# Kernel tuning notes

Measured on AMD Instinct MI355X. Metric: run time of the kernel, lower is better.

Reference implementation:

```python
import jax, jax.numpy as jnp
import numpy as np

ATT_WIDTH = 512  # attention_width from init

def _band_mask(T, width, dtype):
    # tf.matrix_band_part(ones, width//2, (width-1)//2): keep i-j<=lower and j-i<=upper
    lower = width // 2
    upper = (width - 1) // 2
    i = jnp.arange(T)[:, None]
    j = jnp.arange(T)[None, :]
    keep = (i - j <= lower) & (j - i <= upper)
    return keep.astype(dtype)

def setup_inputs() -> dict:
    key = jax.random.key(0)
    k1, k2, k3, k4 = jax.random.split(key, 4)
    B, T, H, D = 8, 2048, 1024, 1024
    scale = 1.0 / np.sqrt(H)  # keep activations sane
    return {
        "inputs": jax.random.normal(k1, (B, T, H), dtype=jnp.float32),
        "WQ": jax.random.normal(k2, (H, D), dtype=jnp.float32) * scale,
        "WK": jax.random.normal(k3, (H, D), dtype=jnp.float32) * scale,
        "WV": jax.random.normal(k4, (H, D), dtype=jnp.float32) * scale,
    }

def reference(inputs, WQ, WK, WV) -> jnp.ndarray:
    B, T, H = inputs.shape
    D = WQ.shape[1]
    scale = jnp.asarray(D, inputs.dtype) ** 0.5
    q = jnp.einsum('bth,hd->btd', inputs, WQ)
    k = jnp.einsum('bth,hd->btd', inputs, WK)
    v = jnp.einsum('bth,hd->btd', inputs, WV)
    score = jnp.einsum('bqd,bkd->bqk', q, k) / scale  # [B,T,T]
    # NOTE: original multiplies score by the 0/1 band mask BEFORE softmax
    # (masked entries become 0, not -inf). Faithful reproduction.
    local = _band_mask(T, ATT_WIDTH, score.dtype)
    score = score * local[None, :, :]
    attn = jax.nn.softmax(score, axis=-1)
    return jnp.einsum('bqk,bkd->bqd', attn, v)
```

## Files before the change

kernel.cpp:

```cpp
#include <hip/hip_runtime.h>
#include <hip/hip_bf16.h>
#include <stdint.h>

typedef __attribute__((ext_vector_type(8))) short bf16x8;
typedef __attribute__((ext_vector_type(4))) short short4v;
typedef __attribute__((ext_vector_type(4))) float f32x4;

#define DEV static __device__ __forceinline__

DEV float bf2f(short u) {
    union { float f; uint32_t i; } c; c.i = ((uint32_t)(uint16_t)u) << 16; return c.f;
}
DEV short f2bf(float f) {
    union { float f; uint32_t i; } c; c.f = f;
    uint32_t i = c.i;
    uint32_t r = i + 0x7FFFu + ((i >> 16) & 1u);
    return (short)(r >> 16);
}

DEV void gload_lds16(const short* g, short* l) {
    __builtin_amdgcn_global_load_lds(
        (const __attribute__((address_space(1))) void*)g,
        (__attribute__((address_space(3))) void*)l,
        16, 0, 0);
}

__global__ __launch_bounds__(256)
void cvt_f32_bf16(const float* __restrict__ in, short* __restrict__ out) {
    long i = ((long)blockIdx.x * 256 + threadIdx.x) * 8;
    float4 a = *(const float4*)&in[i];
    float4 b = *(const float4*)&in[i + 4];
    bf16x8 o;
    o[0] = f2bf(a.x); o[1] = f2bf(a.y); o[2] = f2bf(a.z); o[3] = f2bf(a.w);
    o[4] = f2bf(b.x); o[5] = f2bf(b.y); o[6] = f2bf(b.z); o[7] = f2bf(b.w);
    *(bf16x8*)&out[i] = o;
}

__global__ __launch_bounds__(256)
void transpose_w(const float* __restrict__ W, short* __restrict__ Wt) {
    const int HD = 1024;
    __shared__ float tile[32][33];
    int bx = blockIdx.x, by = blockIdx.y;
    int tx = threadIdx.x & 31, ty = threadIdx.x >> 5;
    #pragma unroll
    for (int r = ty; r < 32; r += 8)
        tile[r][tx] = W[(long)(by * 32 + r) * HD + bx * 32 + tx];
    __syncthreads();
    #pragma unroll
    for (int r = ty; r < 32; r += 8)
        Wt[(long)(bx * 32 + r) * HD + by * 32 + tx] = f2bf(tile[tx][r]);
}


DEV void stage_half(const short* __restrict__ src, int ld, short* dst, int tid) {
    int rr = tid >> 3;
    int cs = ((tid & 7) ^ (rr & 7)) << 3;
    short* d = dst + ((tid >> 6) << 9);
    gload_lds16(src + (long)rr * ld + cs, d);
    gload_lds16(src + (long)(rr + 64) * ld + cs, d + 4096);
}

DEV bf16x8 ld_frag(const short* half, int rowbase, int ks, int lane) {
    int row = rowbase + (lane & 15);
    int idx = (row << 6) + ks * 32 + ((lane >> 4) << 3);
    idx ^= (lane & 7) << 3;
    return *(const bf16x8*)&half[idx];
}

#define SB   __builtin_amdgcn_s_barrier()
#define SCHED0 __builtin_amdgcn_sched_barrier(0)
#define LGK0 do { asm volatile("s_waitcnt lgkmcnt(0)" ::: "memory"); SCHED0; } while (0)
#define VM(n) asm volatile("s_waitcnt vmcnt(" #n ")" ::: "memory")
#define PRIO1 __builtin_amdgcn_s_setprio(1)
#define PRIO0 __builtin_amdgcn_s_setprio(0)

#define READ_A(HP, QM)                                                          \
    do { _Pragma("unroll") for (int iq = 0; iq < 4; ++iq)                       \
         _Pragma("unroll") for (int ks = 0; ks < 2; ++ks)                       \
             ra[iq][ks] = ld_frag(HP, (QM)*64 + iq*16, ks, lane); } while (0)

#define READ_B(HP, QN)                                                          \
    do { _Pragma("unroll") for (int jn = 0; jn < 2; ++jn)                       \
         _Pragma("unroll") for (int ks = 0; ks < 2; ++ks)                       \
             rb[QN][jn][ks] = ld_frag(HP, wn1*64 + (QN)*32 + jn*16, ks, lane); } while (0)

#define MFMA_Q(QM, QN)                                                          \
    do { _Pragma("unroll") for (int iq = 0; iq < 4; ++iq)                       \
         _Pragma("unroll") for (int jn = 0; jn < 2; ++jn)                       \
         _Pragma("unroll") for (int ks = 0; ks < 2; ++ks)                       \
             acc[(QM)*4+iq][(QN)*2+jn] = __builtin_amdgcn_mfma_f32_16x16x32_bf16( \
                 ra[iq][ks], rb[QN][jn][ks], acc[(QM)*4+iq][(QN)*2+jn], 0,0,0); } while (0)

template<int EPI>
__global__ __launch_bounds__(512, 2)
void gemm256(const short* __restrict__ Abase, const short* __restrict__ Bbase,
             void* __restrict__ o0, void* __restrict__ o1, void* __restrict__ o2,
             const float* __restrict__ Crow, const float* __restrict__ Vsum)
{
    const int T = 2048, HD = 1024;
    __shared__ __align__(16) short lds[2][2][2][8192];

    const int tid  = threadIdx.x;
    const int lane = tid & 63;
    const int w    = tid >> 6;
    const int wm   = w >> 2;
    const int wn   = w & 3;
    const int wn1  = wn & 1;
    const int bz   = blockIdx.z;

    int m0, n0, klo, khi, ldA, ldB;
    const short *A, *B;
    if (EPI == 0) {
        m0 = blockIdx.y * 256; n0 = blockIdx.x * 256;
        klo = 0; khi = 1024; ldA = HD; ldB = HD;
        A = Abase; B = Bbase;
    } else if (EPI == 1) {
        int mb = blockIdx.y, kb = mb + (int)blockIdx.x - 1;
        if (kb < 0 || kb > 7) return;
        m0 = mb * 256; n0 = kb * 256;
        klo = 0; khi = 1024; ldA = HD; ldB = HD;
        A = Abase + (long)bz * T * HD; B = Bbase + (long)bz * T * HD;
    } else {
        int mb = blockIdx.y;
        m0 = mb * 256; n0 = blockIdx.x * 256;
        klo = max(m0 - 256, 0); khi = min(m0 + 512, T);
        ldA = T; ldB = T;
        A = Abase + (long)bz * T * T; B = Bbase + (long)bz * HD * T;
    }

    const short* Asrc = A + (long)m0 * ldA + klo;
    const short* Bsrc = B + (long)n0 * ldB + klo;
    const short* hA0 = &lds[0][0][wm][0];
    const short* hA1 = &lds[1][0][wm][0];
    const short* hB0 = &lds[0][1][wn >> 1][0];
    const short* hB1 = &lds[1][1][wn >> 1][0];

    auto stA = [&](int bf, int hf, int t) {
        stage_half(Asrc + (long)hf * 128 * ldA + t * 64, ldA, (short*)&lds[bf][0][hf][0], tid); };
    auto stB = [&](int bf, int hf, int t) {
        stage_half(Bsrc + (long)hf * 128 * ldB + t * 64, ldB, (short*)&lds[bf][1][hf][0], tid); };

    f32x4 acc[8][4];
    #pragma unroll
    for (int i = 0; i < 8; ++i)
        #pragma unroll
        for (int j = 0; j < 4; ++j) { acc[i][j][0]=0.f; acc[i][j][1]=0.f; acc[i][j][2]=0.f; acc[i][j][3]=0.f; }
    bf16x8 ra[4][2];
    bf16x8 rb[2][2][2];

    const int NT = (khi - klo) >> 6;

    stB(0,0,0); stB(0,1,0); stA(0,0,0); stA(0,1,0); stB(1,0,1); stB(1,1,1);
    SCHED0; VM(4); SB;

    for (int i = 0; i < NT/2 - 1; ++i) {
        int t1 = 2*i+1, t2 = 2*i+2, t3 = 2*i+3;
        READ_A(hA0,0); READ_B(hB0,0); stA(1,0,t1); SCHED0; SB; LGK0; PRIO1; MFMA_Q(0,0); PRIO0; SB; SCHED0;
        READ_B(hB0,1); stA(1,1,t1); SCHED0; SB; LGK0; PRIO1; MFMA_Q(0,1); PRIO0; SB; SCHED0;
        READ_A(hA0,1); stB(0,0,t2); SCHED0; SB; LGK0; PRIO1; MFMA_Q(1,1); PRIO0; SB; SCHED0;
        stB(0,1,t2); SCHED0; SB; LGK0; PRIO1; MFMA_Q(1,0); PRIO0; VM(4); SB; SCHED0;
        READ_A(hA1,0); READ_B(hB1,0); stA(0,0,t2); SCHED0; SB; LGK0; PRIO1; MFMA_Q(0,0); PRIO0; SB; SCHED0;
        READ_B(hB1,1); stA(0,1,t2); SCHED0; SB; LGK0; PRIO1; MFMA_Q(0,1); PRIO0; SB; SCHED0;
        READ_A(hA1,1); stB(1,0,t3); SCHED0; SB; LGK0; PRIO1; MFMA_Q(1,1); PRIO0; SB; SCHED0;
        stB(1,1,t3); SCHED0; SB; LGK0; PRIO1; MFMA_Q(1,0); PRIO0; VM(4); SB; SCHED0;
    }
    {
        int t1 = NT - 1;
        READ_A(hA0,0); READ_B(hB0,0); stA(1,0,t1); SCHED0; SB; LGK0; PRIO1; MFMA_Q(0,0); PRIO0; SB; SCHED0;
        READ_B(hB0,1); stA(1,1,t1); SCHED0; SB; LGK0; PRIO1; MFMA_Q(0,1); PRIO0; SB; SCHED0;
        READ_A(hA0,1); SCHED0; SB; LGK0; PRIO1; MFMA_Q(1,1); PRIO0; SB; SCHED0;
        SB; LGK0; PRIO1; MFMA_Q(1,0); PRIO0; VM(0); SB; SCHED0;
        READ_A(hA1,0); READ_B(hB1,0); SCHED0; SB; LGK0; PRIO1; MFMA_Q(0,0); PRIO0; SB; SCHED0;
        READ_B(hB1,1); SCHED0; SB; LGK0; PRIO1; MFMA_Q(0,1); PRIO0; SB; SCHED0;
        READ_A(hA1,1); SCHED0; SB; LGK0; PRIO1; MFMA_Q(1,1); PRIO0; SB; SCHED0;
        SB; LGK0; PRIO1; MFMA_Q(1,0); PRIO0;
    }

    const int fr = lane & 15, fq = lane >> 4;
    const int rbase = m0 + wm * 128, cbase = n0 + wn * 64;

    if (EPI == 0) {
        const int wsel = n0 >> 10;
        if (wsel < 2) {
            short* dst = (short*)(wsel ? o1 : o0);
            #pragma unroll
            for (int mi = 0; mi < 8; ++mi)
                #pragma unroll
                for (int ni = 0; ni < 4; ++ni)
                    #pragma unroll
                    for (int r = 0; r < 4; ++r) {
                        int row = rbase + mi * 16 + fq * 4 + r;
                        int col = (cbase + ni * 16 + fr) & 1023;
                        dst[(long)row * HD + col] = f2bf(acc[mi][ni][r]);
                    }
        } else {
            short* Vt = (short*)o2;
            #pragma unroll
            for (int mi = 0; mi < 8; ++mi)
                #pragma unroll
                for (int ni = 0; ni < 4; ++ni) {
                    int col  = (cbase + ni * 16 + fr) & 1023;
                    int row0 = rbase + mi * 16 + fq * 4;
                    int b = row0 >> 11, t = row0 & 2047;
                    short4v v;
                    #pragma unroll
                    for (int r = 0; r < 4; ++r) v[r] = f2bf(acc[mi][ni][r]);
                    *(short4v*)&Vt[((long)b * HD + col) * T + t] = v;
                }
        }
    } else if (EPI == 1) {
        short* S = (short*)o0 + (long)bz * T * T;
        #pragma unroll
        for (int mi = 0; mi < 8; ++mi)
            #pragma unroll
            for (int ni = 0; ni < 4; ++ni)
                #pragma unroll
                for (int r = 0; r < 4; ++r) {
                    int i = rbase + mi * 16 + fq * 4 + r;
                    int j = cbase + ni * 16 + fr;
                    bool keep = (i - j <= 256) && (j - i <= 255);
                    S[(long)i * T + j] = f2bf(keep ? acc[mi][ni][r] * (1.f/32.f) : 0.f);
                }
    } else {
        float* out = (float*)o0;
        #pragma unroll
        for (int mi = 0; mi < 8; ++mi)
            #pragma unroll
            for (int r = 0; r < 4; ++r) {
                int i = rbase + mi * 16 + fq * 4 + r;
                float ci = Crow[bz * T + i];
                #pragma unroll
                for (int ni = 0; ni < 4; ++ni) {
                    int col = cbase + ni * 16 + fr;
                    out[((long)bz * T + i) * HD + col] = acc[mi][ni][r] + ci * Vsum[bz * HD + col];
                }
            }
    }
}

__global__ __launch_bounds__(256)
void softmax_band(short* __restrict__ S, float* __restrict__ Crow) {
    const int T = 2048;
    int wid = (int)blockIdx.x * 4 + (threadIdx.x >> 6);
    int lane = threadIdx.x & 63;
    int b = wid >> 11, t = wid & 2047;
    int mb = t >> 7;
    int tlo = max(mb - 2, 0) * 128;
    int thi = min(mb + 2, 15) * 128 + 128;
    int nvec = (thi - tlo) >> 3;
    short* row = S + ((long)b * T + t) * T + tlo;

    bool h0 = lane < nvec;
    bool h1 = lane + 64 < nvec;
    bf16x8 v0, v1;
    float f0[8], f1[8];
    float m = 0.f;
    if (h0) {
        v0 = *(const bf16x8*)&row[lane * 8];
        #pragma unroll
        for (int j = 0; j < 8; ++j) { f0[j] = bf2f(v0[j]); m = fmaxf(m, f0[j]); }
    }
    if (h1) {
        v1 = *(const bf16x8*)&row[(lane + 64) * 8];
        #pragma unroll
        for (int j = 0; j < 8; ++j) { f1[j] = bf2f(v1[j]); m = fmaxf(m, f1[j]); }
    }
    #pragma unroll
    for (int o = 32; o; o >>= 1) m = fmaxf(m, __shfl_xor(m, o));

    float e0[8], e1[8];
    float sum = 0.f;
    if (h0) {
        #pragma unroll
        for (int j = 0; j < 8; ++j) { e0[j] = __expf(f0[j] - m); sum += e0[j]; }
    }
    if (h1) {
        #pragma unroll
        for (int j = 0; j < 8; ++j) { e1[j] = __expf(f1[j] - m); sum += e1[j]; }
    }
    #pragma unroll
    for (int o = 32; o; o >>= 1) sum += __shfl_xor(sum, o);
    float em = __expf(-m);
    sum += (float)(2048 - nvec * 8) * em;
    float inv = 1.f / sum;
    float c = em * inv;

    if (h0) {
        #pragma unroll
        for (int j = 0; j < 8; ++j) v0[j] = f2bf(e0[j] * inv - c);
        *(bf16x8*)&row[lane * 8] = v0;
    }
    if (h1) {
        #pragma unroll
        for (int j = 0; j < 8; ++j) v1[j] = f2bf(e1[j] * inv - c);
        *(bf16x8*)&row[(lane + 64) * 8] = v1;
    }
    if (lane == 0) Crow[wid] = c;
}

__global__ __launch_bounds__(256)
void vsum_rows(const short* __restrict__ Vt, float* __restrict__ Vsum) {
    int rowid = (int)blockIdx.x * 4 + (threadIdx.x >> 6);
    int lane = threadIdx.x & 63;
    const short* r = Vt + (long)rowid * 2048;
    float s = 0.f;
    #pragma unroll
    for (int v = 0; v < 4; ++v) {
        bf16x8 x = *(const bf16x8*)&r[(lane + v * 64) * 8];
        #pragma unroll
        for (int j = 0; j < 8; ++j) s += bf2f(x[j]);
    }
    #pragma unroll
    for (int o = 32; o; o >>= 1) s += __shfl_xor(s, o);
    if (lane == 0) Vsum[rowid] = s;
}

extern "C" void kernel_launch(void* const* d_in, const int* in_sizes, int n_in,
                              void* d_out, int out_size, void* d_ws, size_t ws_size,
                              hipStream_t stream) {
    const int B = 8, T = 2048, H = 1024, D = 1024;
    const long MT = (long)B * T;

    const float* X  = (const float*)d_in[0];
    const float* WQ = (const float*)d_in[1];
    const float* WK = (const float*)d_in[2];
    const float* WV = (const float*)d_in[3];
    float* out = (float*)d_out;

    char* ws = (char*)d_ws;
    size_t off = 0;
    auto alloc = [&](size_t bytes) {
        char* p = ws + off;
        off += (bytes + 255) & ~(size_t)255;
        return p;
    };
    short* Xb   = (short*)alloc(MT * H * 2);
    short* Wt   = (short*)alloc(3L * D * H * 2);
    short* Qb   = (short*)alloc(MT * D * 2);
    short* Kb   = (short*)alloc(MT * D * 2);
    short* Vt   = (short*)alloc((long)B * D * T * 2);
    short* S    = (short*)alloc((long)B * T * T * 2);
    float* Crow = (float*)alloc(MT * 4);
    float* Vsum = (float*)alloc((long)B * D * 4);
    if (off > ws_size) return;

    cvt_f32_bf16<<<(int)(MT * H / 2048), 256, 0, stream>>>(X, Xb);
    transpose_w<<<dim3(32, 32), 256, 0, stream>>>(WQ, Wt);
    transpose_w<<<dim3(32, 32), 256, 0, stream>>>(WK, Wt + (long)D * H);
    transpose_w<<<dim3(32, 32), 256, 0, stream>>>(WV, Wt + 2L * D * H);

    gemm256<0><<<dim3(12, 64, 1), 512, 0, stream>>>(Xb, Wt, Qb, Kb, Vt, nullptr, nullptr);

    vsum_rows<<<(int)(B * D / 4), 256, 0, stream>>>(Vt, Vsum);

    gemm256<1><<<dim3(3, 8, B), 512, 0, stream>>>(Qb, Kb, S, nullptr, nullptr, nullptr, nullptr);

    softmax_band<<<(int)(MT / 4), 256, 0, stream>>>(S, Crow);

    gemm256<2><<<dim3(4, 8, B), 512, 0, stream>>>(S, Vt, out, nullptr, nullptr, Crow, Vsum);
}
```

Baseline: 254.3 us.

## Halve barriers in GEMM pipeline and remap blocks for XCD-aware scheduling

Rewrites the main loop schedule so each quarter-step uses one barrier instead of two. B fragments for the next quadrant are prefetched before the barrier, and partial lgkmcnt/vmcnt waits let LDS reads overlap MFMAs. It also remaps linear block IDs so blocks sharing a batch or tile land on the same XCD (p&7), aiming for better L2 reuse. The finer waits and swapped MFMA quadrant order add risk of LDS races if the counts are wrong.

```diff
diff --git a/kernel.cpp b/kernel.cpp
--- a/kernel.cpp
+++ b/kernel.cpp
@@ -67,10 +67,10 @@
     return *(const bf16x8*)&half[idx];
 }
 
-#define SB   __builtin_amdgcn_s_barrier()
 #define SCHED0 __builtin_amdgcn_sched_barrier(0)
-#define LGK0 do { asm volatile("s_waitcnt lgkmcnt(0)" ::: "memory"); SCHED0; } while (0)
-#define VM(n) asm volatile("s_waitcnt vmcnt(" #n ")" ::: "memory")
+#define SBAR do { SCHED0; __builtin_amdgcn_s_barrier(); SCHED0; } while (0)
+#define LGK(n) do { asm volatile("s_waitcnt lgkmcnt(" #n ")" ::: "memory"); SCHED0; } while (0)
+#define VM(n)  do { asm volatile("s_waitcnt vmcnt(" #n ")" ::: "memory"); SCHED0; } while (0)
 #define PRIO1 __builtin_amdgcn_s_setprio(1)
 #define PRIO0 __builtin_amdgcn_s_setprio(0)
 
@@ -106,23 +106,28 @@
     const int wm   = w >> 2;
     const int wn   = w & 3;
     const int wn1  = wn & 1;
-    const int bz   = blockIdx.z;
-
-    int m0, n0, klo, khi, ldA, ldB;
+
+    int m0, n0, klo, khi, ldA, ldB, bz;
     const short *A, *B;
     if (EPI == 0) {
-        m0 = blockIdx.y * 256; n0 = blockIdx.x * 256;
-        klo = 0; khi = 1024; ldA = HD; ldB = HD;
+        int p = (int)blockIdx.x + 12 * (int)blockIdx.y;
+        int lid = (p & 7) * 96 + (p >> 3);
+        m0 = (lid / 12) * 256; n0 = (lid % 12) * 256;
+        klo = 0; khi = 1024; ldA = HD; ldB = HD; bz = 0;
         A = Abase; B = Bbase;
     } else if (EPI == 1) {
-        int mb = blockIdx.y, kb = mb + (int)blockIdx.x - 1;
+        int p = (int)blockIdx.x + 3 * ((int)blockIdx.y + 8 * (int)blockIdx.z);
+        bz = p & 7; int rem = p >> 3;
+        int mb = rem / 3, kb = mb + rem % 3 - 1;
         if (kb < 0 || kb > 7) return;
         m0 = mb * 256; n0 = kb * 256;
         klo = 0; khi = 1024; ldA = HD; ldB = HD;
         A = Abase + (long)bz * T * HD; B = Bbase + (long)bz * T * HD;
     } else {
-        int mb = blockIdx.y;
-        m0 = mb * 256; n0 = blockIdx.x * 256;
+        int p = (int)blockIdx.x + 4 * ((int)blockIdx.y + 8 * (int)blockIdx.z);
+        bz = p & 7; int rem = p >> 3;
+        int mb = rem / 4;
+        m0 = mb * 256; n0 = (rem % 4) * 256;
         klo = max(m0 - 256, 0); khi = min(m0 + 512, T);
         ldA = T; ldB = T;
         A = Abase + (long)bz * T * T; B = Bbase + (long)bz * HD * T;
@@ -151,29 +156,40 @@
     const int NT = (khi - klo) >> 6;
 
     stB(0,0,0); stB(0,1,0); stA(0,0,0); stA(0,1,0); stB(1,0,1); stB(1,1,1);
-    SCHED0; VM(4); SB;
-
+    SCHED0; VM(4); SBAR;
+    READ_B(hB0, 0); SCHED0;
+
+    #pragma unroll 1
     for (int i = 0; i < NT/2 - 1; ++i) {
         int t1 = 2*i+1, t2 = 2*i+2, t3 = 2*i+3;
-        READ_A(hA0,0); READ_B(hB0,0); stA(1,0,t1); SCHED0; SB; LGK0; PRIO1; MFMA_Q(0,0); PRIO0; SB; SCHED0;
-        READ_B(hB0,1); stA(1,1,t1); SCHED0; SB; LGK0; PRIO1; MFMA_Q(0,1); PRIO0; SB; SCHED0;
-        READ_A(hA0,1); stB(0,0,t2); SCHED0; SB; LGK0; PRIO1; MFMA_Q(1,1); PRIO0; SB; SCHED0;
-        stB(0,1,t2); SCHED0; SB; LGK0; PRIO1; MFMA_Q(1,0); PRIO0; VM(4); SB; SCHED0;
-        READ_A(hA1,0); READ_B(hB1,0); stA(0,0,t2); SCHED0; SB; LGK0; PRIO1; MFMA_Q(0,0); PRIO0; SB; SCHED0;
-        READ_B(hB1,1); stA(0,1,t2); SCHED0; SB; LGK0; PRIO1; MFMA_Q(0,1); PRIO0; SB; SCHED0;
-        READ_A(hA1,1); stB(1,0,t3); SCHED0; SB; LGK0; PRIO1; MFMA_Q(1,1); PRIO0; SB; SCHED0;
-        stB(1,1,t3); SCHED0; SB; LGK0; PRIO1; MFMA_Q(1,0); PRIO0; VM(4); SB; SCHED0;
+        SBAR; READ_A(hA0,0); SCHED0; READ_B(hB0,1); SCHED0; stA(1,0,t1);
+        LGK(4); PRIO1; MFMA_Q(0,0); PRIO0; SCHED0;
+        SBAR; stA(1,1,t1); LGK(0); PRIO1; MFMA_Q(0,1); PRIO0; SCHED0;
+        SBAR; READ_A(hA0,1); SCHED0; stB(0,0,t2); LGK(0);
+        PRIO1; MFMA_Q(1,0); PRIO0; SCHED0; VM(2); SCHED0;
+        SBAR; READ_B(hB1,0); SCHED0; stB(0,1,t2);
+        PRIO1; MFMA_Q(1,1); PRIO0; SCHED0;
+        SBAR; READ_A(hA1,0); SCHED0; READ_B(hB1,1); SCHED0; stA(0,0,t2);
+        LGK(4); PRIO1; MFMA_Q(0,0); PRIO0; SCHED0;
+        SBAR; stA(0,1,t2); LGK(0); PRIO1; MFMA_Q(0,1); PRIO0; SCHED0;
+        SBAR; READ_A(hA1,1); SCHED0; stB(1,0,t3); LGK(0);
+        PRIO1; MFMA_Q(1,0); PRIO0; SCHED0; VM(2); SCHED0;
+        SBAR; READ_B(hB0,0); SCHED0; stB(1,1,t3);
+        PRIO1; MFMA_Q(1,1); PRIO0; SCHED0;
     }
     {
         int t1 = NT - 1;
-        READ_A(hA0,0); READ_B(hB0,0); stA(1,0,t1); SCHED0; SB; LGK0; PRIO1; MFMA_Q(0,0); PRIO0; SB; SCHED0;
-        READ_B(hB0,1); stA(1,1,t1); SCHED0; SB; LGK0; PRIO1; MFMA_Q(0,1); PRIO0; SB; SCHED0;
-        READ_A(hA0,1); SCHED0; SB; LGK0; PRIO1; MFMA_Q(1,1); PRIO0; SB; SCHED0;
-        SB; LGK0; PRIO1; MFMA_Q(1,0); PRIO0; VM(0); SB; SCHED0;
-        READ_A(hA1,0); READ_B(hB1,0); SCHED0; SB; LGK0; PRIO1; MFMA_Q(0,0); PRIO0; SB; SCHED0;
-        READ_B(hB1,1); SCHED0; SB; LGK0; PRIO1; MFMA_Q(0,1); PRIO0; SB; SCHED0;
-        READ_A(hA1,1); SCHED0; SB; LGK0; PRIO1; MFMA_Q(1,1); PRIO0; SB; SCHED0;
-        SB; LGK0; PRIO1; MFMA_Q(1,0); PRIO0;
+        SBAR; READ_A(hA0,0); SCHED0; READ_B(hB0,1); SCHED0; stA(1,0,t1);
+        LGK(4); PRIO1; MFMA_Q(0,0); PRIO0; SCHED0;
+        SBAR; stA(1,1,t1); LGK(0); PRIO1; MFMA_Q(0,1); PRIO0; SCHED0;
+        SBAR; READ_A(hA0,1); SCHED0; LGK(0);
+        PRIO1; MFMA_Q(1,0); PRIO0; SCHED0; VM(0); SCHED0;
+        SBAR; READ_B(hB1,0); SCHED0; PRIO1; MFMA_Q(1,1); PRIO0; SCHED0;
+        SBAR; READ_A(hA1,0); SCHED0; READ_B(hB1,1); SCHED0;
+        LGK(4); PRIO1; MFMA_Q(0,0); PRIO0; SCHED0;
+        SBAR; LGK(0); PRIO1; MFMA_Q(0,1); PRIO0; SCHED0;
+        SBAR; READ_A(hA1,1); SCHED0; LGK(0); PRIO1; MFMA_Q(1,0); PRIO0; SCHED0;
+        SBAR; PRIO1; MFMA_Q(1,1); PRIO0; SCHED0;
     }
 
     const int fr = lane & 15, fq = lane >> 4;
```

Result: faster. 236.9 us (-6.9%).
